# Optimization experiments

Hardware: AMD Instinct MI355X
Metric: run time of the kernel (lower is better)

## Reference

```python
import jax, jax.numpy as jnp
import numpy as np


def setup_inputs() -> dict:
    key = jax.random.key(0)
    k1, k2, k3, k4 = jax.random.split(key, 4)
    B, H, W, K = 2, 768, 768, 8
    colors = jax.random.uniform(k1, (B, H, W, K, 4), dtype=jnp.float32)
    # label channel holds integer human ids encoded as floats (as sampled from textures)
    labels = jax.random.randint(k2, (B, H, W, K), 0, K).astype(jnp.float32)
    texels = jnp.concatenate([colors, labels[..., None]], axis=-1)  # (B,H,W,K,5)
    zbuf = jax.random.normal(k3, (B, H, W, K), dtype=jnp.float32) + 0.5
    bkg_color = jax.random.uniform(k4, (3,), dtype=jnp.float32)
    return {"texels": texels, "zbuf": zbuf, "bkg_color": bkg_color}


def reference(texels, zbuf, bkg_color):
    B, H, W, K, _ = texels.shape
    colors = texels[..., :4]          # (B,H,W,K,4) rgba
    labels = texels[..., 4]           # (B,H,W,K) float-encoded label
    valid = zbuf >= 0                 # labels were set to nan / -1 where zbuf < 0

    # ---- back-to-front alpha compositing over the K depth layers (k = K-1 .. 0) ----
    xs = (
        jnp.moveaxis(colors[..., :3], 3, 0)[::-1],  # layer_color (K,B,H,W,3)
        jnp.moveaxis(colors[..., 3], 3, 0)[::-1],   # layer_alpha (K,B,H,W)
        jnp.moveaxis(zbuf, 3, 0)[::-1],             # layer_depth
        jnp.moveaxis(labels, 3, 0)[::-1],           # layer_label
        jnp.moveaxis(valid, 3, 0)[::-1],            # label validity
    )
    rgb0 = jnp.broadcast_to(bkg_color, (B, H, W, 3)).astype(texels.dtype)
    a0 = jnp.zeros((B, H, W), texels.dtype)
    d0 = jnp.full((B, H, W), 100.0, texels.dtype)       # composite_depth init
    l0 = jnp.full((B, H, W), float(K), texels.dtype)    # composite_label init

    def step(carry, x):
        rgb, a, d, l = carry
        lc, la, ld, ll, v = x
        rgb = lc * la[..., None] + rgb * (1.0 - la[..., None])
        a = jnp.maximum(la, a)
        d = jnp.where(ld > 0, ld * la + d * (1.0 - la), d)
        l = jnp.where(v, jnp.where(la > 0.5, ll, l), l)
        return (rgb, a, d, l), None

    (rgb, a, d, l), _ = jax.lax.scan(step, (rgb0, a0, d0, l0), xs)
    composite_image = jnp.concatenate([rgb, a[..., None]], axis=-1)  # (B,H,W,4)
    composite_depth = d                                              # (B,H,W)
    composite_label = jnp.where(l > K - 0.5, -1.0, l)
    composite_label = jnp.round(composite_label).astype(jnp.int64)   # (B,H,W)

    # ---- raster_each_labeled_human: first-hit gather per label ----
    N = K
    labels_int = jnp.where(valid, jnp.round(labels).astype(jnp.int32), -1)  # (B,H,W,K)
    hit = labels_int[..., None] == jnp.arange(N, dtype=jnp.int32)           # (B,H,W,K,N)
    hit = jnp.concatenate([hit, jnp.ones((B, H, W, 1, N), bool)], axis=3)   # sentinel row
    first = jnp.argmax(hit, axis=3)                                         # (B,H,W,N)
    colors_void = jnp.concatenate(
        [colors, jnp.zeros((B, H, W, 1, 4), colors.dtype)], axis=3)         # (B,H,W,K+1,4)
    gathered = jnp.take_along_axis(colors_void, first[..., None], axis=3)   # (B,H,W,N,4)
    hrgb, ha = gathered[..., :3], gathered[..., 3:4]
    human_images = jnp.concatenate([hrgb * ha + bkg_color * (1.0 - ha), ha], axis=-1)

    return composite_image, composite_depth, composite_label, human_images
```

## Files before the change

kernel.cpp:

```cpp
#include <hip/hip_runtime.h>


#define TW  40
#define HWD 36

typedef float vf4 __attribute__((ext_vector_type(4)));

__device__ __forceinline__ int slotOf(int f4, int p) {
    return (f4 < 8) ? (f4 ^ (p & 7)) : (8 + ((f4 - 8) ^ (p & 1)));
}

__global__ __launch_bounds__(256, 4) void composer_kernel(
    const float* __restrict__ texels,
    const float* __restrict__ zbuf,
    const float* __restrict__ bkg,
    float* __restrict__ out,
    int npix)
{
    __shared__ float lds[256 * TW];

    const int tid  = threadIdx.x;
    const int base = blockIdx.x * 256;
    const bool full = (base + 256 <= npix);
    const int pix  = base + tid;
    const bool active = (pix < npix);
    const float bk0 = bkg[0], bk1 = bkg[1], bk2 = bkg[2];
    const size_t np = (size_t)npix;

    float t[40];
    float z[8];

    if (active) {
        const float4* zp = reinterpret_cast<const float4*>(zbuf + (size_t)pix * 8);
        float4 v0 = zp[0], v1 = zp[1];
        z[0]=v0.x; z[1]=v0.y; z[2]=v0.z; z[3]=v0.w;
        z[4]=v1.x; z[5]=v1.y; z[6]=v1.z; z[7]=v1.w;
    }

    if (full) {
        const float4* gt = reinterpret_cast<const float4*>(texels) + (size_t)base * 10;
        #pragma unroll
        for (int i = 0; i < 10; ++i) {
            int idx = i * 256 + tid;
            float4 v = gt[idx];
            int p  = idx / 10;
            int f4 = idx % 10;
            *reinterpret_cast<float4*>(&lds[p * TW + slotOf(f4, p) * 4]) = v;
        }
        __syncthreads();

        #pragma unroll
        for (int f4 = 0; f4 < 10; ++f4) {
            float4 v = *reinterpret_cast<const float4*>(&lds[tid * TW + slotOf(f4, tid) * 4]);
            t[4*f4+0]=v.x; t[4*f4+1]=v.y; t[4*f4+2]=v.z; t[4*f4+3]=v.w;
        }
        __syncthreads();
    } else if (active) {
        const float4* tp = reinterpret_cast<const float4*>(texels + (size_t)pix * 40);
        #pragma unroll
        for (int i = 0; i < 10; ++i) {
            float4 v = tp[i];
            t[4*i+0]=v.x; t[4*i+1]=v.y; t[4*i+2]=v.z; t[4*i+3]=v.w;
        }
    }

    if (active) {
        float r = bk0, g = bk1, b = bk2;
        float a = 0.0f, d = 100.0f, l = 8.0f;
        #pragma unroll
        for (int k = 7; k >= 0; --k) {
            const float lr = t[5*k+0], lg = t[5*k+1], lb = t[5*k+2];
            const float la = t[5*k+3], ll = t[5*k+4];
            const float zd = z[k];
            const float om = 1.0f - la;
            r = fmaf(lr, la, r * om);
            g = fmaf(lg, la, g * om);
            b = fmaf(lb, la, b * om);
            a = fmaxf(la, a);
            if (zd > 0.0f)  d = fmaf(zd, la, d * om);
            if (zd >= 0.0f) l = (la > 0.5f) ? ll : l;
        }

        {
            vf4 img = { r, g, b, a };
            __builtin_nontemporal_store(img, reinterpret_cast<vf4*>(out) + pix);
            __builtin_nontemporal_store(d, out + np*4 + pix);
            const float lo = (l > 7.5f) ? -1.0f : (float)__float2int_rn(l);
            __builtin_nontemporal_store(lo, out + np*5 + pix);
        }

        int li[8];
        #pragma unroll
        for (int k = 0; k < 8; ++k)
            li[k] = (z[k] >= 0.0f) ? __float2int_rn(t[5*k+4]) : -1;

        if (full) {
            float* hb = &lds[tid * HWD];
            #pragma unroll
            for (int n = 0; n < 8; ++n) {
                float cr=0.f, cg=0.f, cb=0.f, ca=0.f; bool found=false;
                #pragma unroll
                for (int k = 0; k < 8; ++k) {
                    bool m = (!found) && (li[k] == n);
                    if (m) { cr=t[5*k+0]; cg=t[5*k+1]; cb=t[5*k+2]; ca=t[5*k+3]; found=true; }
                }
                const float oma = 1.0f - ca;
                *reinterpret_cast<float4*>(&hb[n*4]) =
                    make_float4(fmaf(cr, ca, bk0 * oma),
                                fmaf(cg, ca, bk1 * oma),
                                fmaf(cb, ca, bk2 * oma),
                                ca);
            }
        } else {
            vf4* o_h = reinterpret_cast<vf4*>(out + np*6) + (size_t)pix * 8;
            #pragma unroll
            for (int n = 0; n < 8; ++n) {
                float cr=0.f, cg=0.f, cb=0.f, ca=0.f; bool found=false;
                #pragma unroll
                for (int k = 0; k < 8; ++k) {
                    bool m = (!found) && (li[k] == n);
                    if (m) { cr=t[5*k+0]; cg=t[5*k+1]; cb=t[5*k+2]; ca=t[5*k+3]; found=true; }
                }
                const float oma = 1.0f - ca;
                vf4 h = { fmaf(cr,ca,bk0*oma), fmaf(cg,ca,bk1*oma),
                          fmaf(cb,ca,bk2*oma), ca };
                __builtin_nontemporal_store(h, o_h + n);
            }
        }
    }

    if (full) {
        __syncthreads();
        vf4* gh = reinterpret_cast<vf4*>(out + np*6) + (size_t)base * 8;
        #pragma unroll
        for (int i = 0; i < 8; ++i) {
            int idx = i * 256 + tid;
            int P = idx >> 3;
            int c = idx & 7;
            float4 s = *reinterpret_cast<const float4*>(&lds[P * HWD + c * 4]);
            vf4 h = { s.x, s.y, s.z, s.w };
            __builtin_nontemporal_store(h, gh + idx);
        }
    }
}

extern "C" void kernel_launch(void* const* d_in, const int* in_sizes, int n_in,
                              void* d_out, int out_size, void* d_ws, size_t ws_size,
                              hipStream_t stream) {
    const float* texels = (const float*)d_in[0];
    const float* zbuf   = (const float*)d_in[1];
    const float* bkg    = (const float*)d_in[2];
    float* out = (float*)d_out;

    const int npix = in_sizes[1] / 8;
    const int blocks = (npix + 255) / 256;
    hipLaunchKernelGGL(composer_kernel, dim3(blocks), dim3(256), 0, stream,
                       texels, zbuf, bkg, out, npix);
}
```

Baseline: 69.90 us.

## Convert to persistent grid-stride kernel with register prefetch of next tile

```diff
diff --git a/kernel.cpp b/kernel.cpp
--- a/kernel.cpp
+++ b/kernel.cpp
@@ -10,7 +10,13 @@
     return (f4 < 8) ? (f4 ^ (p & 7)) : (8 + ((f4 - 8) ^ (p & 1)));
 }
 
-__global__ __launch_bounds__(256, 4) void composer_kernel(
+__device__ __forceinline__ void sync_lgkm() {
+    asm volatile("s_waitcnt lgkmcnt(0)" ::: "memory");
+    __builtin_amdgcn_s_barrier();
+    __builtin_amdgcn_sched_barrier(0);
+}
+
+__global__ __launch_bounds__(256) void composer_kernel(
     const float* __restrict__ texels,
     const float* __restrict__ zbuf,
     const float* __restrict__ bkg,
@@ -19,99 +25,172 @@
 {
     __shared__ float lds[256 * TW];
 
-    const int tid  = threadIdx.x;
-    const int base = blockIdx.x * 256;
-    const bool full = (base + 256 <= npix);
-    const int pix  = base + tid;
-    const bool active = (pix < npix);
+    const int tid   = threadIdx.x;
+    const int nfull = npix >> 8;
     const float bk0 = bkg[0], bk1 = bkg[1], bk2 = bkg[2];
     const size_t np = (size_t)npix;
 
-    float t[40];
-    float z[8];
-
-    if (active) {
-        const float4* zp = reinterpret_cast<const float4*>(zbuf + (size_t)pix * 8);
-        float4 v0 = zp[0], v1 = zp[1];
-        z[0]=v0.x; z[1]=v0.y; z[2]=v0.z; z[3]=v0.w;
-        z[4]=v1.x; z[5]=v1.y; z[6]=v1.z; z[7]=v1.w;
-    }
-
-    if (full) {
-        const float4* gt = reinterpret_cast<const float4*>(texels) + (size_t)base * 10;
-        #pragma unroll
-        for (int i = 0; i < 10; ++i) {
-            int idx = i * 256 + tid;
-            float4 v = gt[idx];
-            int p  = idx / 10;
-            int f4 = idx % 10;
-            *reinterpret_cast<float4*>(&lds[p * TW + slotOf(f4, p) * 4]) = v;
+    int tile = blockIdx.x;
+    if (tile < nfull) {
+        float4 pf[10];
+        float4 pz0, pz1;
+        {
+            const float4* gt = reinterpret_cast<const float4*>(texels) + (size_t)tile * 2560;
+            #pragma unroll
+            for (int i = 0; i < 10; ++i) pf[i] = gt[i * 256 + tid];
+            const float4* zp = reinterpret_cast<const float4*>(zbuf) + (((size_t)tile << 8) + tid) * 2;
+            pz0 = zp[0]; pz1 = zp[1];
         }
-        __syncthreads();
-
-        #pragma unroll
-        for (int f4 = 0; f4 < 10; ++f4) {
-            float4 v = *reinterpret_cast<const float4*>(&lds[tid * TW + slotOf(f4, tid) * 4]);
-            t[4*f4+0]=v.x; t[4*f4+1]=v.y; t[4*f4+2]=v.z; t[4*f4+3]=v.w;
-        }
-        __syncthreads();
-    } else if (active) {
-        const float4* tp = reinterpret_cast<const float4*>(texels + (size_t)pix * 40);
-        #pragma unroll
-        for (int i = 0; i < 10; ++i) {
-            float4 v = tp[i];
-            t[4*i+0]=v.x; t[4*i+1]=v.y; t[4*i+2]=v.z; t[4*i+3]=v.w;
+
+        while (true) {
+            const int base     = tile << 8;
+            const int pix      = base + tid;
+            const int nexttile = tile + (int)gridDim.x;
+            const bool havenext = (nexttile < nfull);
+
+            sync_lgkm();
+
+            #pragma unroll
+            for (int i = 0; i < 10; ++i) {
+                int idx = i * 256 + tid;
+                int p = idx / 10, f4 = idx - 10 * p;
+                *reinterpret_cast<float4*>(&lds[p * TW + slotOf(f4, p) * 4]) = pf[i];
+            }
+
+            float z[8] = { pz0.x, pz0.y, pz0.z, pz0.w, pz1.x, pz1.y, pz1.z, pz1.w };
+
+            if (havenext) {
+                const float4* gt = reinterpret_cast<const float4*>(texels) + (size_t)nexttile * 2560;
+                #pragma unroll
+                for (int i = 0; i < 10; ++i) pf[i] = gt[i * 256 + tid];
+                const float4* zp = reinterpret_cast<const float4*>(zbuf) + (((size_t)nexttile << 8) + tid) * 2;
+                pz0 = zp[0]; pz1 = zp[1];
+            }
+
+            sync_lgkm();
+
+            float t[40];
+            #pragma unroll
+            for (int f4 = 0; f4 < 10; ++f4) {
+                float4 v = *reinterpret_cast<const float4*>(&lds[tid * TW + slotOf(f4, tid) * 4]);
+                t[4*f4+0]=v.x; t[4*f4+1]=v.y; t[4*f4+2]=v.z; t[4*f4+3]=v.w;
+            }
+
+            float r = bk0, g = bk1, b = bk2;
+            float a = 0.0f, d = 100.0f, l = 8.0f;
+            #pragma unroll
+            for (int k = 7; k >= 0; --k) {
+                const float lr = t[5*k+0], lg = t[5*k+1], lb = t[5*k+2];
+                const float la = t[5*k+3], ll = t[5*k+4];
+                const float zd = z[k];
+                const float om = 1.0f - la;
+                r = fmaf(lr, la, r * om);
+                g = fmaf(lg, la, g * om);
+                b = fmaf(lb, la, b * om);
+                a = fmaxf(la, a);
+                if (zd > 0.0f)  d = fmaf(zd, la, d * om);
+                if (zd >= 0.0f) l = (la > 0.5f) ? ll : l;
+            }
+
+            {
+                vf4 img = { r, g, b, a };
+                __builtin_nontemporal_store(img, reinterpret_cast<vf4*>(out) + pix);
+                __builtin_nontemporal_store(d, out + np*4 + pix);
+                const float lo = (l > 7.5f) ? -1.0f : (float)__float2int_rn(l);
+                __builtin_nontemporal_store(lo, out + np*5 + pix);
+            }
+
+            int li[8];
+            #pragma unroll
+            for (int k = 0; k < 8; ++k)
+                li[k] = (z[k] >= 0.0f) ? __float2int_rn(t[5*k+4]) : -1;
+
+            float4 hv[8];
+            #pragma unroll
+            for (int n = 0; n < 8; ++n) {
+                float cr=0.f, cg=0.f, cb=0.f, ca=0.f; bool found=false;
+                #pragma unroll
+                for (int k = 0; k < 8; ++k) {
+                    bool m = (!found) && (li[k] == n);
+                    if (m) { cr=t[5*k+0]; cg=t[5*k+1]; cb=t[5*k+2]; ca=t[5*k+3]; found=true; }
+                }
+                const float oma = 1.0f - ca;
+                hv[n] = make_float4(fmaf(cr, ca, bk0 * oma),
+                                    fmaf(cg, ca, bk1 * oma),
+                                    fmaf(cb, ca, bk2 * oma),
+                                    ca);
+            }
+
+            sync_lgkm();
+
+            {
+                float* hb = &lds[tid * HWD];
+                #pragma unroll
+                for (int n = 0; n < 8; ++n)
+                    *reinterpret_cast<float4*>(&hb[n*4]) = hv[n];
+            }
+
+            sync_lgkm();
+
+            {
+                vf4* gh = reinterpret_cast<vf4*>(out + np*6) + (size_t)base * 8;
+                #pragma unroll
+                for (int i = 0; i < 8; ++i) {
+                    int idx = i * 256 + tid;
+                    int P = idx >> 3, c = idx & 7;
+                    float4 s = *reinterpret_cast<const float4*>(&lds[P * HWD + c * 4]);
+                    vf4 h = { s.x, s.y, s.z, s.w };
+                    __builtin_nontemporal_store(h, gh + idx);
+                }
+            }
+
+            if (!havenext) break;
+            tile = nexttile;
         }
     }
 
-    if (active) {
-        float r = bk0, g = bk1, b = bk2;
-        float a = 0.0f, d = 100.0f, l = 8.0f;
-        #pragma unroll
-        for (int k = 7; k >= 0; --k) {
-            const float lr = t[5*k+0], lg = t[5*k+1], lb = t[5*k+2];
-            const float la = t[5*k+3], ll = t[5*k+4];
-            const float zd = z[k];
-            const float om = 1.0f - la;
-            r = fmaf(lr, la, r * om);
-            g = fmaf(lg, la, g * om);
-            b = fmaf(lb, la, b * om);
-            a = fmaxf(la, a);
-            if (zd > 0.0f)  d = fmaf(zd, la, d * om);
-            if (zd >= 0.0f) l = (la > 0.5f) ? ll : l;
-        }
-
-        {
+    const int rem = npix & 255;
+    if (rem && (int)blockIdx.x == (nfull % (int)gridDim.x)) {
+        const int pix = (nfull << 8) + tid;
+        if (pix < npix) {
+            float t[40]; float z[8];
+            const float4* tp = reinterpret_cast<const float4*>(texels + (size_t)pix * 40);
+            #pragma unroll
+            for (int i = 0; i < 10; ++i) {
+                float4 v = tp[i];
+                t[4*i+0]=v.x; t[4*i+1]=v.y; t[4*i+2]=v.z; t[4*i+3]=v.w;
+            }
+            const float4* zp = reinterpret_cast<const float4*>(zbuf + (size_t)pix * 8);
+            float4 v0 = zp[0], v1 = zp[1];
+            z[0]=v0.x; z[1]=v0.y; z[2]=v0.z; z[3]=v0.w;
+            z[4]=v1.x; z[5]=v1.y; z[6]=v1.z; z[7]=v1.w;
+
+            float r = bk0, g = bk1, b = bk2;
+            float a = 0.0f, d = 100.0f, l = 8.0f;
+            #pragma unroll
+            for (int k = 7; k >= 0; --k) {
+                const float lr = t[5*k+0], lg = t[5*k+1], lb = t[5*k+2];
+                const float la = t[5*k+3], ll = t[5*k+4];
+                const float zd = z[k];
+                const float om = 1.0f - la;
+                r = fmaf(lr, la, r * om);
+                g = fmaf(lg, la, g * om);
+                b = fmaf(lb, la, b * om);
+                a = fmaxf(la, a);
+                if (zd > 0.0f)  d = fmaf(zd, la, d * om);
+                if (zd >= 0.0f) l = (la > 0.5f) ? ll : l;
+            }
             vf4 img = { r, g, b, a };
             __builtin_nontemporal_store(img, reinterpret_cast<vf4*>(out) + pix);
             __builtin_nontemporal_store(d, out + np*4 + pix);
             const float lo = (l > 7.5f) ? -1.0f : (float)__float2int_rn(l);
             __builtin_nontemporal_store(lo, out + np*5 + pix);
-        }
-
-        int li[8];
-        #pragma unroll
-        for (int k = 0; k < 8; ++k)
-            li[k] = (z[k] >= 0.0f) ? __float2int_rn(t[5*k+4]) : -1;
-
-        if (full) {
-            float* hb = &lds[tid * HWD];
-            #pragma unroll
-            for (int n = 0; n < 8; ++n) {
-                float cr=0.f, cg=0.f, cb=0.f, ca=0.f; bool found=false;
-                #pragma unroll
-                for (int k = 0; k < 8; ++k) {
-                    bool m = (!found) && (li[k] == n);
-                    if (m) { cr=t[5*k+0]; cg=t[5*k+1]; cb=t[5*k+2]; ca=t[5*k+3]; found=true; }
-                }
-                const float oma = 1.0f - ca;
-                *reinterpret_cast<float4*>(&hb[n*4]) =
-                    make_float4(fmaf(cr, ca, bk0 * oma),
-                                fmaf(cg, ca, bk1 * oma),
-                                fmaf(cb, ca, bk2 * oma),
-                                ca);
-            }
-        } else {
+
+            int li[8];
+            #pragma unroll
+            for (int k = 0; k < 8; ++k)
+                li[k] = (z[k] >= 0.0f) ? __float2int_rn(t[5*k+4]) : -1;
+
             vf4* o_h = reinterpret_cast<vf4*>(out + np*6) + (size_t)pix * 8;
             #pragma unroll
             for (int n = 0; n < 8; ++n) {
@@ -128,20 +207,6 @@
             }
         }
     }
-
-    if (full) {
-        __syncthreads();
-        vf4* gh = reinterpret_cast<vf4*>(out + np*6) + (size_t)base * 8;
-        #pragma unroll
-        for (int i = 0; i < 8; ++i) {
-            int idx = i * 256 + tid;
-            int P = idx >> 3;
-            int c = idx & 7;
-            float4 s = *reinterpret_cast<const float4*>(&lds[P * HWD + c * 4]);
-            vf4 h = { s.x, s.y, s.z, s.w };
-            __builtin_nontemporal_store(h, gh + idx);
-        }
-    }
 }
 
 extern "C" void kernel_launch(void* const* d_in, const int* in_sizes, int n_in,
@@ -152,8 +217,10 @@
     const float* bkg    = (const float*)d_in[2];
     float* out = (float*)d_out;
 
-    const int npix = in_sizes[1] / 8;
-    const int blocks = (npix + 255) / 256;
+    const int npix   = in_sizes[1] / 8;
+    const int ntiles = (npix + 255) / 256;
+    int blocks = ntiles < 1024 ? ntiles : 1024;
+    if (blocks < 1) blocks = 1;
     hipLaunchKernelGGL(composer_kernel, dim3(blocks), dim3(256), 0, stream,
                        texels, zbuf, bkg, out, npix);
 }
```

Result: slower. 131.6 us (+88.2%).
